# Kernel optimization log

Measured on AMD Instinct MI355X. Metric: run time of the kernel, lower is better.

## Reference

```python
import jax, jax.numpy as jnp
import numpy as np

B, S, D = 2, 2048, 1024
H = 16
HD = D // H  # 64

def setup_inputs() -> dict:
    key = jax.random.key(0)
    ks = jax.random.split(key, 6)
    scale = 0.02
    return {
        "query": jax.random.normal(ks[0], (B, S, D), dtype=jnp.float32),
        "key":   jax.random.normal(ks[1], (B, S, D), dtype=jnp.float32),
        "value": jax.random.normal(ks[2], (B, S, D), dtype=jnp.float32),
        "Wq": jax.random.normal(ks[3], (D, D), dtype=jnp.float32) * scale,
        "bq": jnp.zeros((D,), dtype=jnp.float32),
        "Wk": jax.random.normal(ks[4], (D, D), dtype=jnp.float32) * scale,
        "bk": jnp.zeros((D,), dtype=jnp.float32),
        "Wv": jax.random.normal(ks[5], (D, D), dtype=jnp.float32) * scale,
        "bv": jnp.zeros((D,), dtype=jnp.float32),
    }

def reference(query, key, value, Wq, bq, Wk, bk, Wv, bv):
    b, s, d = query.shape
    # Linear projections (weights stored as (in, out))
    q = query @ Wq + bq   # [B,S,D]
    k = key   @ Wk + bk
    v = value @ Wv + bv
    # split heads -> [B,H,S,HD]
    q = q.reshape(b, s, H, HD).transpose(0, 2, 1, 3)
    k = k.reshape(b, s, H, HD).transpose(0, 2, 1, 3)
    v = v.reshape(b, s, H, HD).transpose(0, 2, 1, 3)
    # scaled dot-product attention (no mask; dropout = identity in eval)
    scores = jnp.einsum("bhqd,bhkd->bhqk", q, k) / jnp.sqrt(jnp.float32(HD))
    attn = jax.nn.softmax(scores, axis=-1)
    out = jnp.einsum("bhqk,bhkd->bhqd", attn, v)
    # merge heads -> [B,S,D]
    return out.transpose(0, 2, 1, 3).reshape(b, s, d)
```

## Files before the change

kernel.cpp:

```cpp
#include <hip/hip_runtime.h>
#include <stdint.h>

#define D_  1024
#define S_  2048
#define B_  2
#define H_  16
#define HD_ 64
#define M_  (B_*S_)
#define KVB 64

typedef unsigned short u16;
typedef __attribute__((ext_vector_type(8)))  __bf16 bf16x8;
typedef __attribute__((ext_vector_type(4)))  float  f32x4;
typedef __attribute__((ext_vector_type(16))) float  f32x16;

__device__ __forceinline__ u16 f2bf(float f) {
    __bf16 h = (__bf16)f;
    union { __bf16 h; u16 u; } x; x.h = h;
    return x.u;
}

__device__ __forceinline__ void gload_lds16(const void* g, void* l) {
    __builtin_amdgcn_global_load_lds(
        (const __attribute__((address_space(1))) uint32_t*)g,
        (__attribute__((address_space(3))) uint32_t*)l, 16, 0, 0);
}

__global__ __launch_bounds__(256) void cvt3_kernel(
    const float* __restrict__ a, const float* __restrict__ b, const float* __restrict__ c,
    u16* __restrict__ oa, u16* __restrict__ ob, u16* __restrict__ oc) {
    const float* in = blockIdx.y == 0 ? a : (blockIdx.y == 1 ? b : c);
    u16* out = blockIdx.y == 0 ? oa : (blockIdx.y == 1 ? ob : oc);
    int i = (blockIdx.x * 256 + threadIdx.x) * 4;
    float4 v = *(const float4*)(in + i);
    ushort4 o;
    o.x = f2bf(v.x); o.y = f2bf(v.y); o.z = f2bf(v.z); o.w = f2bf(v.w);
    *(ushort4*)(out + i) = o;
}

__global__ __launch_bounds__(256) void transpose_w3(
    const float* __restrict__ Wq, const float* __restrict__ Wk, const float* __restrict__ Wv,
    u16* __restrict__ Wtq, u16* __restrict__ Wtk, u16* __restrict__ Wtv) {
    const float* W = blockIdx.z == 0 ? Wq : (blockIdx.z == 1 ? Wk : Wv);
    u16* Wt = blockIdx.z == 0 ? Wtq : (blockIdx.z == 1 ? Wtk : Wtv);
    __shared__ u16 t[64][65];
    int k0 = blockIdx.x * 64, n0 = blockIdx.y * 64;
    int tid = threadIdx.x;
    int c4 = (tid & 15) * 4, r = tid >> 4;
#pragma unroll
    for (int i = 0; i < 4; i++) {
        int row = r + i * 16;
        float4 v = *(const float4*)(W + (uint64_t)(k0 + row) * D_ + n0 + c4);
        t[row][c4 + 0] = f2bf(v.x);
        t[row][c4 + 1] = f2bf(v.y);
        t[row][c4 + 2] = f2bf(v.z);
        t[row][c4 + 3] = f2bf(v.w);
    }
    __syncthreads();
#pragma unroll
    for (int i = 0; i < 4; i++) {
        int nrow = r + i * 16;
        ushort4 o;
        o.x = t[c4 + 0][nrow]; o.y = t[c4 + 1][nrow];
        o.z = t[c4 + 2][nrow]; o.w = t[c4 + 3][nrow];
        *(ushort4*)(Wt + (uint64_t)(n0 + nrow) * D_ + k0 + c4) = o;
    }
}

__global__ __launch_bounds__(256) void gemm_qkv(
    const u16* __restrict__ Xq, const u16* __restrict__ Xk, const u16* __restrict__ Xv,
    const u16* __restrict__ Wtq, const u16* __restrict__ Wtk, const u16* __restrict__ Wtv,
    const float* __restrict__ bq, const float* __restrict__ bk, const float* __restrict__ bv,
    u16* __restrict__ Qo, u16* __restrict__ Ko, u16* __restrict__ Vo)
{
    int p = blockIdx.z;
    const u16* X    = p == 0 ? Xq  : (p == 1 ? Xk  : Xv);
    const u16* Wt   = p == 0 ? Wtq : (p == 1 ? Wtk : Wtv);
    const float* bias = p == 0 ? bq : (p == 1 ? bk : bv);
    u16* out = p == 0 ? Qo : (p == 1 ? Ko : Vo);
    float scale = p == 0 ? 0.125f : 1.0f;

    __shared__ __align__(16) u16 As[128 * 32];
    __shared__ __align__(16) u16 Bs[128 * 32];

    int tid = threadIdx.x;
    int lane = tid & 63, wid = tid >> 6;
    int lrow = lane & 15, lk = lane >> 4;
    int wr = wid >> 1, wc = wid & 1;
    int bm = blockIdx.x, bn = blockIdx.y;

    f32x4 acc[4][4] = {};

    const uint64_t Xrow0 = (uint64_t)bm * 128 * D_;
    const uint64_t Wrow0 = (uint64_t)bn * 128 * D_;

    for (int kt = 0; kt < D_ / 32; ++kt) {
        int k0 = kt * 32;
#pragma unroll
        for (int it = 0; it < 2; ++it) {
            int i = it * 256 + tid;
            int row = i >> 2, cc = i & 3;
            gload_lds16(X  + Xrow0 + (uint64_t)row * D_ + k0 + cc * 8,
                        (char*)As + it * 4096 + wid * 1024);
            gload_lds16(Wt + Wrow0 + (uint64_t)row * D_ + k0 + cc * 8,
                        (char*)Bs + it * 4096 + wid * 1024);
        }
        __syncthreads();
        bf16x8 a[4], b[4];
#pragma unroll
        for (int m = 0; m < 4; m++)
            a[m] = *(const bf16x8*)((const char*)As + (wr * 64 + m * 16 + lrow) * 64 + lk * 16);
#pragma unroll
        for (int n = 0; n < 4; n++)
            b[n] = *(const bf16x8*)((const char*)Bs + (wc * 64 + n * 16 + lrow) * 64 + lk * 16);
        if (p < 2) {
#pragma unroll
            for (int m = 0; m < 4; m++)
#pragma unroll
                for (int n = 0; n < 4; n++)
                    acc[m][n] = __builtin_amdgcn_mfma_f32_16x16x32_bf16(a[m], b[n], acc[m][n], 0, 0, 0);
        } else {
#pragma unroll
            for (int m = 0; m < 4; m++)
#pragma unroll
                for (int n = 0; n < 4; n++)
                    acc[m][n] = __builtin_amdgcn_mfma_f32_16x16x32_bf16(b[n], a[m], acc[m][n], 0, 0, 0);
        }
        __syncthreads();
    }

    if (p < 2) {
#pragma unroll
        for (int m = 0; m < 4; m++) {
            int grow_base = bm * 128 + wr * 64 + m * 16 + lk * 4;
#pragma unroll
            for (int n = 0; n < 4; n++) {
                int gcol = bn * 128 + wc * 64 + n * 16 + lrow;
                float bb = bias[gcol];
                int h = gcol >> 6, hd = gcol & 63;
#pragma unroll
                for (int j = 0; j < 4; j++) {
                    int grow = grow_base + j;
                    int b_ = grow >> 11, s = grow & 2047;
                    out[(((uint64_t)(b_ * H_ + h)) * S_ + s) * HD_ + hd] =
                        f2bf((acc[m][n][j] + bb) * scale);
                }
            }
        }
    } else {
#pragma unroll
        for (int m = 0; m < 4; m++) {
            int sg = bm * 128 + wr * 64 + m * 16 + lrow;
            int b_ = sg >> 11, s = sg & 2047;
#pragma unroll
            for (int n = 0; n < 4; n++) {
                int ch_base = bn * 128 + wc * 64 + n * 16 + lk * 4;
#pragma unroll
                for (int j = 0; j < 4; j++) {
                    int ch = ch_base + j;
                    int h = ch >> 6, hd = ch & 63;
                    out[(((uint64_t)(b_ * H_ + h)) * HD_ + hd) * S_ + s] =
                        f2bf(acc[m][n][j] + bias[ch]);
                }
            }
        }
    }
}

__global__ __launch_bounds__(512) void attn_kernel(
    const u16* __restrict__ Q, const u16* __restrict__ K,
    const u16* __restrict__ VT, float* __restrict__ out)
{
    __shared__ __align__(16) char smem[32768];

    int lin = blockIdx.x;
    int bh = lin & 31, qt = lin >> 5;

    int tid = threadIdx.x;
    int w = tid >> 6, lane = tid & 63;
    int q5 = lane & 31, h = lane >> 5;

    bf16x8 qf[4];
    const u16* Qrow = Q + ((uint64_t)bh * S_ + qt * 256 + w * 32 + q5) * HD_;
#pragma unroll
    for (int kk = 0; kk < 4; kk++)
        qf[kk] = *(const bf16x8*)(Qrow + kk * 16 + h * 8);

    f32x16 o_acc[2] = {};
    float m_run = -1e30f, l_run = 0.f;

    const char* Kbase = (const char*)(K  + (uint64_t)bh * S_ * HD_);
    const char* Vbase = (const char*)(VT + (uint64_t)bh * HD_ * S_);

    int o16 = tid * 16;
    int rr  = o16 >> 7;
    int os  = o16 ^ ((rr & 7) << 4);

    auto stage = [&](int buf, int t) {
        int kv0 = t * KVB;
        gload_lds16(Kbase + (uint64_t)kv0 * 128 + os,
                    smem + buf * 8192 + w * 1024);
        gload_lds16(Vbase + (uint64_t)rr * (S_ * 2) + kv0 * 2 + (os & 127),
                    smem + 16384 + buf * 8192 + w * 1024);
    };

    stage(0, 0);
    __syncthreads();
    int cur = 0;

    const int NT = S_ / KVB;
    for (int t = 0; t < NT; ++t) {
        if (t + 1 < NT) stage(cur ^ 1, t + 1);

        const char* Kc = smem + cur * 8192;
        const char* Vc = smem + 16384 + cur * 8192;
        int sw = (q5 & 7) << 4;

        f32x16 sacc[2] = {};
        __builtin_amdgcn_s_setprio(1);
#pragma unroll
        for (int c = 0; c < 2; c++) {
            int rb = (c * 32 + q5) * 128;
#pragma unroll
            for (int kk = 0; kk < 4; kk++) {
                bf16x8 kf = *(const bf16x8*)(Kc + rb + ((kk * 32 + h * 16) ^ sw));
                sacc[c] = __builtin_amdgcn_mfma_f32_32x32x16_bf16(kf, qf[kk], sacc[c], 0, 0, 0);
            }
        }
        __builtin_amdgcn_s_setprio(0);

        float mp = sacc[0][0];
#pragma unroll
        for (int r = 1; r < 16; r++) mp = fmaxf(mp, sacc[0][r]);
#pragma unroll
        for (int r = 0; r < 16; r++) mp = fmaxf(mp, sacc[1][r]);
        mp = fmaxf(mp, __shfl_xor(mp, 32, 64));
        float mnew = fmaxf(m_run, mp);
        float sc = __expf(m_run - mnew);
        m_run = mnew;

        float ts = 0.f;
#pragma unroll
        for (int c = 0; c < 2; c++)
#pragma unroll
            for (int r = 0; r < 16; r++) {
                float pv = __expf(sacc[c][r] - mnew);
                sacc[c][r] = pv;
                ts += pv;
            }
        ts += __shfl_xor(ts, 32, 64);
        l_run = l_run * sc + ts;
#pragma unroll
        for (int hb = 0; hb < 2; hb++)
#pragma unroll
            for (int r = 0; r < 16; r++) o_acc[hb][r] *= sc;

        bf16x8 pa[4];
#pragma unroll
        for (int ks = 0; ks < 4; ks++) {
            int c = ks >> 1, gg = ks & 1;
            uint32_t a0, a1, b0, b1;
            asm("v_cvt_pk_bf16_f32 %0, %1, %2" : "=v"(a0) : "v"(sacc[c][8*gg+0]), "v"(sacc[c][8*gg+1]));
            asm("v_cvt_pk_bf16_f32 %0, %1, %2" : "=v"(a1) : "v"(sacc[c][8*gg+2]), "v"(sacc[c][8*gg+3]));
            asm("v_cvt_pk_bf16_f32 %0, %1, %2" : "=v"(b0) : "v"(sacc[c][8*gg+4]), "v"(sacc[c][8*gg+5]));
            asm("v_cvt_pk_bf16_f32 %0, %1, %2" : "=v"(b1) : "v"(sacc[c][8*gg+6]), "v"(sacc[c][8*gg+7]));
            asm volatile("v_permlane32_swap_b32 %0, %1" : "+v"(a0), "+v"(b0));
            asm volatile("v_permlane32_swap_b32 %0, %1" : "+v"(a1), "+v"(b1));
            union { uint32_t u[4]; bf16x8 v; } pu;
            pu.u[0] = a0; pu.u[1] = a1; pu.u[2] = b0; pu.u[3] = b1;
            pa[ks] = pu.v;
        }

        __builtin_amdgcn_s_setprio(1);
#pragma unroll
        for (int hb = 0; hb < 2; hb++) {
            int rb = (hb * 32 + q5) * 128;
#pragma unroll
            for (int ks = 0; ks < 4; ks++) {
                bf16x8 vf = *(const bf16x8*)(Vc + rb + ((ks * 32 + h * 16) ^ sw));
                o_acc[hb] = __builtin_amdgcn_mfma_f32_32x32x16_bf16(vf, pa[ks], o_acc[hb], 0, 0, 0);
            }
        }
        __builtin_amdgcn_s_setprio(0);

        __syncthreads();
        cur ^= 1;
    }

    float inv = 1.0f / l_run;
    int b_ = bh >> 4, head = bh & 15;
    int qq = lane >> 1, c0 = (lane & 1) * 16;
    float* scrw = (float*)smem + w * 1024;
    float* orow = out + ((uint64_t)(b_ * S_ + qt * 256 + w * 32 + qq)) * D_ + head * 64;
#pragma unroll
    for (int hb = 0; hb < 2; hb++) {
#pragma unroll
        for (int r = 0; r < 16; r++) {
            int col = (r & 3) + 8 * (r >> 2) + 4 * h;
            scrw[q5 * 32 + (col ^ ((q5 & 7) << 2))] = o_acc[hb][r] * inv;
        }
        __syncthreads();
#pragma unroll
        for (int j = 0; j < 4; j++) {
            int cb = c0 + j * 4;
            float4 val = *(float4*)&scrw[qq * 32 + (cb ^ ((qq & 7) << 2))];
            *(float4*)(orow + hb * 32 + cb) = val;
        }
        __syncthreads();
    }
}

extern "C" void kernel_launch(void* const* d_in, const int* in_sizes, int n_in,
                              void* d_out, int out_size, void* d_ws, size_t ws_size,
                              hipStream_t stream) {
    const float* q  = (const float*)d_in[0];
    const float* k  = (const float*)d_in[1];
    const float* v  = (const float*)d_in[2];
    const float* Wq = (const float*)d_in[3];
    const float* bq = (const float*)d_in[4];
    const float* Wk = (const float*)d_in[5];
    const float* bk = (const float*)d_in[6];
    const float* Wv = (const float*)d_in[7];
    const float* bv = (const float*)d_in[8];
    float* out = (float*)d_out;

    u16* ws = (u16*)d_ws;
    const size_t XN = (size_t)M_ * D_;
    const size_t WN = (size_t)D_ * D_;
    u16* Xq  = ws;          u16* Xk  = Xq  + XN;  u16* Xv  = Xk  + XN;
    u16* Wtq = Xv + XN;     u16* Wtk = Wtq + WN;  u16* Wtv = Wtk + WN;
    u16* Qb  = Wtv + WN;    u16* Kb  = Qb  + XN;  u16* Vb  = Kb  + XN;

    cvt3_kernel<<<dim3(XN / 1024, 3), 256, 0, stream>>>(q, k, v, Xq, Xk, Xv);
    transpose_w3<<<dim3(16, 16, 3), 256, 0, stream>>>(Wq, Wk, Wv, Wtq, Wtk, Wtv);
    gemm_qkv<<<dim3(32, 8, 3), 256, 0, stream>>>(Xq, Xk, Xv, Wtq, Wtk, Wtv,
                                                 bq, bk, bv, Qb, Kb, Vb);
    attn_kernel<<<256, 512, 0, stream>>>(Qb, Kb, Vb, out);
}
```

Measured before the change: 232.5 us.

## Triple-buffer QKV GEMM LDS loads with XOR swizzle to overlap and avoid conflicts

The QKV projection GEMM now uses three LDS buffers and issues direct global-to-LDS loads two k-tiles ahead, waiting with explicit vmcnt counts and a single barrier per iteration. The aim is to hide global load latency behind MFMA work. The column group is also XOR-swizzled by row so the LDS fragment reads avoid bank conflicts. This triples LDS use, which may cut occupancy, and it depends on the manual vmcnt accounting being correct.

```diff
diff --git a/kernel.cpp b/kernel.cpp
--- a/kernel.cpp
+++ b/kernel.cpp
@@ -80,8 +80,8 @@
     u16* out = p == 0 ? Qo : (p == 1 ? Ko : Vo);
     float scale = p == 0 ? 0.125f : 1.0f;
 
-    __shared__ __align__(16) u16 As[128 * 32];
-    __shared__ __align__(16) u16 Bs[128 * 32];
+    __shared__ __align__(16) u16 As[3][128 * 32];
+    __shared__ __align__(16) u16 Bs[3][128 * 32];
 
     int tid = threadIdx.x;
     int lane = tid & 63, wid = tid >> 6;
@@ -94,25 +94,41 @@
     const uint64_t Xrow0 = (uint64_t)bm * 128 * D_;
     const uint64_t Wrow0 = (uint64_t)bn * 128 * D_;
 
-    for (int kt = 0; kt < D_ / 32; ++kt) {
+    auto stage = [&](int buf, int kt) {
         int k0 = kt * 32;
 #pragma unroll
         for (int it = 0; it < 2; ++it) {
             int i = it * 256 + tid;
-            int row = i >> 2, cc = i & 3;
-            gload_lds16(X  + Xrow0 + (uint64_t)row * D_ + k0 + cc * 8,
-                        (char*)As + it * 4096 + wid * 1024);
-            gload_lds16(Wt + Wrow0 + (uint64_t)row * D_ + k0 + cc * 8,
-                        (char*)Bs + it * 4096 + wid * 1024);
-        }
-        __syncthreads();
+            int row = i >> 2;
+            int cg = (i & 3) ^ ((row >> 1) & 3);
+            gload_lds16(X  + Xrow0 + (uint64_t)row * D_ + k0 + cg * 8,
+                        (char*)As[buf] + it * 4096 + wid * 1024);
+            gload_lds16(Wt + Wrow0 + (uint64_t)row * D_ + k0 + cg * 8,
+                        (char*)Bs[buf] + it * 4096 + wid * 1024);
+        }
+    };
+
+    stage(0, 0);
+    stage(1, 1);
+    asm volatile("s_waitcnt vmcnt(4)" ::: "memory");
+    __builtin_amdgcn_s_barrier();
+
+    const int NKT = D_ / 32;
+    for (int kt = 0; kt < NKT; ++kt) {
+        int cur = kt % 3;
+        if (kt + 2 < NKT) stage((kt + 2) % 3, kt + 2);
+
         bf16x8 a[4], b[4];
 #pragma unroll
-        for (int m = 0; m < 4; m++)
-            a[m] = *(const bf16x8*)((const char*)As + (wr * 64 + m * 16 + lrow) * 64 + lk * 16);
-#pragma unroll
-        for (int n = 0; n < 4; n++)
-            b[n] = *(const bf16x8*)((const char*)Bs + (wc * 64 + n * 16 + lrow) * 64 + lk * 16);
+        for (int m = 0; m < 4; m++) {
+            int r = wr * 64 + m * 16 + lrow;
+            a[m] = *(const bf16x8*)((const char*)As[cur] + r * 64 + ((lk ^ ((r >> 1) & 3)) * 16));
+        }
+#pragma unroll
+        for (int n = 0; n < 4; n++) {
+            int r = wc * 64 + n * 16 + lrow;
+            b[n] = *(const bf16x8*)((const char*)Bs[cur] + r * 64 + ((lk ^ ((r >> 1) & 3)) * 16));
+        }
         if (p < 2) {
 #pragma unroll
             for (int m = 0; m < 4; m++)
@@ -126,7 +142,14 @@
                 for (int n = 0; n < 4; n++)
                     acc[m][n] = __builtin_amdgcn_mfma_f32_16x16x32_bf16(b[n], a[m], acc[m][n], 0, 0, 0);
         }
-        __syncthreads();
+
+        if (kt + 1 < NKT) {
+            if (kt + 2 < NKT)
+                asm volatile("s_waitcnt vmcnt(4)" ::: "memory");
+            else
+                asm volatile("s_waitcnt vmcnt(0)" ::: "memory");
+            __builtin_amdgcn_s_barrier();
+        }
     }
 
     if (p < 2) {
```

After: 237.7 us. 1.02x slower.
